# Optimization experiments

Measured on AMD Instinct MI355X. Metric: run time of the kernel, lower is better.

The kernel has to match this reference:

```python
import jax, jax.numpy as jnp
import numpy as np

B = 1024      # graphs
NODES = 128   # nodes per graph (uniform -> batch_ptr = arange(B+1)*NODES)
IN = 64
HID = 256
OUT = 128
NBLK = 3
TAU = 0.25


def _ln(x, g, b):
    # LayerNorm over last dim, eps=1e-5 (torch default)
    mu = jnp.mean(x, axis=-1, keepdims=True)
    var = jnp.mean((x - mu) ** 2, axis=-1, keepdims=True)
    return (x - mu) / jnp.sqrt(var + 1e-5) * g + b


def setup_inputs() -> dict:
    key = jax.random.key(0)
    ks = jax.random.split(key, 4)
    sc = 0.05
    return {
        "H": jax.random.normal(ks[0], (B * NODES, IN), jnp.float32),
        "batch_ptr": jnp.arange(B + 1, dtype=jnp.int32) * NODES,
        # ResNetMLP params: stem Linear(IN->HID)+LN, NBLK residual blocks
        # Linear(HID->HID)+LN+ReLU, head Linear(HID->OUT)+LN (last_norm=True).
        "W_in": jax.random.normal(ks[1], (IN, HID), jnp.float32) * sc,
        "b_in": jnp.zeros((HID,), jnp.float32),
        "g_in": jnp.ones((HID,), jnp.float32),
        "beta_in": jnp.zeros((HID,), jnp.float32),
        "Wb": jax.random.normal(ks[2], (NBLK, HID, HID), jnp.float32) * sc,
        "bb": jnp.zeros((NBLK, HID), jnp.float32),
        "gb": jnp.ones((NBLK, HID), jnp.float32),
        "betab": jnp.zeros((NBLK, HID), jnp.float32),
        "W_out": jax.random.normal(ks[3], (HID, OUT), jnp.float32) * sc,
        "b_out": jnp.zeros((OUT,), jnp.float32),
        "g_out": jnp.ones((OUT,), jnp.float32),
        "beta_out": jnp.zeros((OUT,), jnp.float32),
    }


def reference(H, batch_ptr, W_in, b_in, g_in, beta_in, Wb, bb, gb, betab,
              W_out, b_out, g_out, beta_out):
    # ResNetMLP projection (dropout is identity in eval)
    x = jax.nn.relu(_ln(H @ W_in + b_in, g_in, beta_in))          # [N, HID]
    for k in range(NBLK):
        x = x + jax.nn.relu(_ln(x @ Wb[k] + bb[k], gb[k], betab[k]))
    z = _ln(x @ W_out + b_out, g_out, beta_out)                   # [N, OUT]

    # Uniform-size graphs: ragged per-graph loop vectorizes to [Bg, n, OUT]
    Bg = batch_ptr.shape[0] - 1
    n = H.shape[0] // Bg
    z3 = z.reshape(Bg, n, OUT)

    # s_i = mean_j ||z_i - z_j||_2 (includes j=i, distance 0)
    sq = jnp.sum(z3 * z3, axis=-1)                                # [Bg, n]
    d2 = sq[:, :, None] + sq[:, None, :] - 2.0 * jnp.einsum("bid,bjd->bij", z3, z3)
    d = jnp.sqrt(jnp.maximum(d2, 0.0) + 1e-12)                    # [Bg, n, n]
    s = jnp.mean(d, axis=-1)                                      # [Bg, n]

    w = jax.nn.softmax(s / TAU, axis=-1)                          # [Bg, n]
    v_loc = jnp.einsum("bi,bid->bd", w, z3)                       # [Bg, OUT]
    return v_loc, w
```

## Files before the change

### kernel.cpp

```cpp
#include <hip/hip_runtime.h>
#include <stdint.h>


typedef __attribute__((ext_vector_type(8))) short bf16x8;
typedef __attribute__((ext_vector_type(4))) float f32x4;

#define XB_STRIDE 264
#define ZB_STRIDE 136

__device__ __forceinline__ unsigned int rne16(float f) {
  unsigned int u = __builtin_bit_cast(unsigned int, f);
  return u + 0x7fffu + ((u >> 16) & 1u);
}
__device__ __forceinline__ unsigned short f2bf(float f) {
  return (unsigned short)(rne16(f) >> 16);
}
__device__ __forceinline__ float bf2f(unsigned short h) {
  unsigned int u = ((unsigned int)h) << 16;
  return __builtin_bit_cast(float, u);
}
__device__ __forceinline__ f32x4 zero4() {
  f32x4 v; v.x = 0.f; v.y = 0.f; v.z = 0.f; v.w = 0.f; return v;
}
__device__ __forceinline__ unsigned int pack_pair(float v) {
  unsigned int t = rne16(v);
  unsigned int tp = (unsigned int)__builtin_amdgcn_update_dpp(
      0, (int)t, 0xB1, 0xF, 0xF, true);
  return __builtin_amdgcn_perm(tp, t, 0x07060302);
}
template <int CTRL>
__device__ __forceinline__ float dpp_add(float v) {
  int p = __builtin_amdgcn_update_dpp(0, __builtin_bit_cast(int, v),
                                      CTRL, 0xF, 0xF, true);
  return v + __builtin_bit_cast(float, p);
}
__device__ __forceinline__ float red16(float v) {
  v = dpp_add<0xB1>(v);
  v = dpp_add<0x4E>(v);
  v = dpp_add<0x141>(v);
  v = dpp_add<0x140>(v);
  return v;
}

__global__ void prep_weights(const float* __restrict__ Win, const float* __restrict__ Wb,
                             const float* __restrict__ Wout, unsigned short* __restrict__ ws) {
  int g = blockIdx.x * 256 + threadIdx.x;
  if (g >= 30720) return;
  const float* W; int N; int local;
  if (g < 2048) { W = Win; N = 256; local = g; }
  else if (g < 26624) {
    int i = g - 2048; int blk = i >> 13; local = i & 8191;
    W = Wb + blk * 65536; N = 256;
  } else { W = Wout; N = 128; local = g - 26624; }
  int f = local >> 6, lane = local & 63;
  int NTL = N >> 4;
  int kc = f / NTL, ntile = f - kc * NTL;
  int n = ntile * 16 + (lane & 15);
  int k0 = kc * 32 + (lane >> 4) * 8;
  unsigned short o[8];
#pragma unroll
  for (int e = 0; e < 8; ++e) o[e] = f2bf(W[(size_t)(k0 + e) * N + n]);
  *reinterpret_cast<uint4*>(ws + (size_t)g * 8) = *reinterpret_cast<uint4*>(o);
}

template <int KL, int N, int MODE>
__device__ __forceinline__ void layer(unsigned short* __restrict__ Xb,
                                      float* __restrict__ statQ, float* __restrict__ muR,
                                      const unsigned short* __restrict__ Wf,
                                      int tid, int wave, int lane,
                                      const float* __restrict__ bias,
                                      const float* __restrict__ gam,
                                      const float* __restrict__ bet,
                                      f32x4 (&xprev)[2][2]) {
  constexpr int NT = N / 128;
  constexpr int NTL = N / 16;
  constexpr int KC = KL / 32;
  const int q = lane >> 4, l16 = lane & 15;
  const int colbase = wave * 16 * NT;
  const unsigned short* Wl = Wf + lane * 8;

  float bcol[NT], gcol[NT], becol[NT];
#pragma unroll
  for (int nt = 0; nt < NT; ++nt) {
    int col = colbase + 16 * nt + l16;
    bcol[nt] = bias[col]; gcol[nt] = gam[col]; becol[nt] = bet[col];
  }
  f32x4 acc[2][NT];
#pragma unroll
  for (int mt = 0; mt < 2; ++mt)
#pragma unroll
    for (int nt = 0; nt < NT; ++nt) acc[mt][nt] = zero4();

  bf16x8 bcur[NT];
#pragma unroll
  for (int nt = 0; nt < NT; ++nt)
    bcur[nt] = *reinterpret_cast<const bf16x8*>(Wl + (size_t)(wave * NT + nt) * 512);

  __syncthreads();
#pragma unroll
  for (int kc = 0; kc < KC; ++kc) {
    bf16x8 bnext[NT];
    if (kc + 1 < KC) {
#pragma unroll
      for (int nt = 0; nt < NT; ++nt)
        bnext[nt] = *reinterpret_cast<const bf16x8*>(
            Wl + (size_t)((kc + 1) * NTL + wave * NT + nt) * 512);
    }
    const int kk = kc * 32 + q * 8;
    bf16x8 a0 = *reinterpret_cast<const bf16x8*>(Xb + l16 * XB_STRIDE + kk);
    bf16x8 a1 = *reinterpret_cast<const bf16x8*>(Xb + (16 + l16) * XB_STRIDE + kk);
#pragma unroll
    for (int nt = 0; nt < NT; ++nt)
      acc[0][nt] = __builtin_amdgcn_mfma_f32_16x16x32_bf16(a0, bcur[nt], acc[0][nt], 0, 0, 0);
#pragma unroll
    for (int nt = 0; nt < NT; ++nt)
      acc[1][nt] = __builtin_amdgcn_mfma_f32_16x16x32_bf16(a1, bcur[nt], acc[1][nt], 0, 0, 0);
    if (kc + 1 < KC) {
#pragma unroll
      for (int nt = 0; nt < NT; ++nt) bcur[nt] = bnext[nt];
    }
  }

#pragma unroll
  for (int mt = 0; mt < 2; ++mt) {
#pragma unroll
    for (int nt = 0; nt < NT; ++nt) {
      acc[mt][nt].x += bcol[nt]; acc[mt][nt].y += bcol[nt];
      acc[mt][nt].z += bcol[nt]; acc[mt][nt].w += bcol[nt];
    }
    f32x4 s1 = acc[mt][0];
    f32x4 s2 = acc[mt][0] * acc[mt][0];
    if constexpr (NT == 2) { s1 += acc[mt][1]; s2 += acc[mt][1] * acc[mt][1]; }
#pragma unroll
    for (int r = 0; r < 4; ++r) { s1[r] = red16(s1[r]); s2[r] = red16(s2[r]); }
    if (l16 == 0) {
      float* sp = statQ + wave * 68 + mt * 32 + q * 8;
      f32x4 v0, v1;
      v0.x = s1.x; v0.y = s2.x; v0.z = s1.y; v0.w = s2.y;
      v1.x = s1.z; v1.y = s2.z; v1.z = s1.w; v1.w = s2.w;
      *reinterpret_cast<f32x4*>(sp) = v0;
      *reinterpret_cast<f32x4*>(sp + 4) = v1;
    }
  }
  __syncthreads();
  if (tid < 32) {
    float S1 = 0.f, S2 = 0.f;
#pragma unroll
    for (int w = 0; w < 8; ++w) {
      float2 v = *reinterpret_cast<const float2*>(statQ + w * 68 + 2 * tid);
      S1 += v.x; S2 += v.y;
    }
    float mu = S1 * (1.0f / N);
    float var = S2 * (1.0f / N) - mu * mu;
    float rstd = rsqrtf(var + 1e-5f);
    float2 o; o.x = mu; o.y = rstd;
    *reinterpret_cast<float2*>(muR + 2 * tid) = o;
  }
  __syncthreads();
  unsigned int* Xw = reinterpret_cast<unsigned int*>(Xb);
#pragma unroll
  for (int mt = 0; mt < 2; ++mt)
#pragma unroll
    for (int r = 0; r < 4; ++r) {
      const int row = 16 * mt + 4 * q + r;
      float2 m = *reinterpret_cast<const float2*>(muR + 2 * row);
      const float nmr = -m.x * m.y;
#pragma unroll
      for (int nt = 0; nt < NT; ++nt) {
        float z = __builtin_fmaf(acc[mt][nt][r], m.y, nmr);
        float o = __builtin_fmaf(z, gcol[nt], becol[nt]);
        float xv;
        if constexpr (MODE == 0) { xv = fmaxf(o, 0.f); xprev[mt][nt][r] = xv; }
        else if constexpr (MODE == 1) {
          xv = xprev[mt][nt][r] + fmaxf(o, 0.f); xprev[mt][nt][r] = xv;
        } else { xv = o; }
        unsigned int pk = pack_pair(xv);
        if ((l16 & 1) == 0)
          Xw[row * 132 + ((colbase + 16 * nt + l16) >> 1)] = pk;
      }
    }
}

__global__ __attribute__((amdgpu_flat_work_group_size(512, 512), amdgpu_waves_per_eu(4)))
void mlp_main(const float* __restrict__ H, const unsigned short* __restrict__ ws,
              const float* __restrict__ b_in, const float* __restrict__ g_in,
              const float* __restrict__ beta_in,
              const float* __restrict__ bb, const float* __restrict__ gb,
              const float* __restrict__ betab,
              const float* __restrict__ b_out, const float* __restrict__ g_out,
              const float* __restrict__ beta_out,
              unsigned short* __restrict__ Z) {
  __shared__ __attribute__((aligned(16))) unsigned short Xb[32 * XB_STRIDE];
  __shared__ __attribute__((aligned(16))) float statQ[8 * 68];
  __shared__ __attribute__((aligned(16))) float muR[64];
  const int tid = threadIdx.x;
  const int wave = tid >> 6, lane = tid & 63;

  {
    int row = tid >> 4, c4 = (tid & 15) * 4;
    float4 f = *reinterpret_cast<const float4*>(
        H + ((size_t)blockIdx.x * 32 + row) * 64 + c4);
    unsigned int t0 = rne16(f.x), t1 = rne16(f.y), t2 = rne16(f.z), t3 = rne16(f.w);
    uint2 o;
    o.x = __builtin_amdgcn_perm(t1, t0, 0x07060302);
    o.y = __builtin_amdgcn_perm(t3, t2, 0x07060302);
    *reinterpret_cast<uint2*>(Xb + row * XB_STRIDE + c4) = o;
  }

  f32x4 xprev[2][2];
  layer<64, 256, 0>(Xb, statQ, muR, ws,           tid, wave, lane, b_in,     g_in,     beta_in,  xprev);
  layer<256, 256, 1>(Xb, statQ, muR, ws + 16384,  tid, wave, lane, bb,       gb,       betab,    xprev);
  layer<256, 256, 1>(Xb, statQ, muR, ws + 81920,  tid, wave, lane, bb + 256, gb + 256, betab + 256, xprev);
  layer<256, 256, 1>(Xb, statQ, muR, ws + 147456, tid, wave, lane, bb + 512, gb + 512, betab + 512, xprev);
  layer<256, 128, 2>(Xb, statQ, muR, ws + 212992, tid, wave, lane, b_out,    g_out,    beta_out, xprev);
  __syncthreads();

  {
    int row = tid >> 4, c8 = (tid & 15) * 8;
    uint4 v = *reinterpret_cast<const uint4*>(Xb + row * XB_STRIDE + c8);
    *reinterpret_cast<uint4*>(Z + ((size_t)blockIdx.x * 32 + row) * 128 + c8) = v;
  }
}

__global__ __attribute__((amdgpu_flat_work_group_size(512, 512)))
void pool_main(const unsigned short* __restrict__ Z, float* __restrict__ out) {
  __shared__ unsigned short Zb[128 * ZB_STRIDE];
  __shared__ float sqv[128], sm[128], smw[128];
  const int tid = threadIdx.x;
  const int g = blockIdx.x;
  const int wave = tid >> 6, lane = tid & 63;
  const int q = lane >> 4, l16 = lane & 15;

  {
    int zr = tid >> 2, zc = (tid & 3) * 32;
    const uint4* zp = reinterpret_cast<const uint4*>(Z + ((size_t)g * 128 + zr) * 128 + zc);
    uint4* zd = reinterpret_cast<uint4*>(Zb + zr * ZB_STRIDE + zc);
    zd[0] = zp[0]; zd[1] = zp[1]; zd[2] = zp[2]; zd[3] = zp[3];
  }
  __syncthreads();

  f32x4 g2[8];
#pragma unroll
  for (int nt = 0; nt < 8; ++nt) g2[nt] = zero4();
#pragma unroll
  for (int ks = 0; ks < 4; ++ks) {
    int kk = ks * 32 + q * 8;
    bf16x8 a = *reinterpret_cast<const bf16x8*>(Zb + (16 * wave + l16) * ZB_STRIDE + kk);
#pragma unroll
    for (int nt = 0; nt < 8; ++nt) {
      bf16x8 bfr = *reinterpret_cast<const bf16x8*>(Zb + (16 * nt + l16) * ZB_STRIDE + kk);
      g2[nt] = __builtin_amdgcn_mfma_f32_16x16x32_bf16(a, bfr, g2[nt], 0, 0, 0);
    }
  }
  if ((l16 >> 2) == q) {
#pragma unroll
    for (int nt = 0; nt < 8; ++nt)
      if (nt == wave) {
#pragma unroll
        for (int r = 0; r < 4; ++r)
          if ((l16 & 3) == r) sqv[16 * wave + l16] = g2[nt][r];
      }
  }
  __syncthreads();
  float sqi[4];
#pragma unroll
  for (int r = 0; r < 4; ++r) sqi[r] = sqv[16 * wave + q * 4 + r];
  float sp[4] = {0.f, 0.f, 0.f, 0.f};
#pragma unroll
  for (int nt = 0; nt < 8; ++nt) {
    float sqj = sqv[16 * nt + l16];
#pragma unroll
    for (int r = 0; r < 4; ++r) {
      float d2 = sqi[r] + sqj - 2.0f * g2[nt][r];
      sp[r] += sqrtf(fmaxf(d2, 0.f) + 1e-12f);
    }
  }
#pragma unroll
  for (int d = 1; d < 16; d <<= 1) {
#pragma unroll
    for (int r = 0; r < 4; ++r) { float t = sp[r]; t += __shfl_xor(t, d); sp[r] = t; }
  }
  if (l16 == 0) {
#pragma unroll
    for (int r = 0; r < 4; ++r) sm[16 * wave + q * 4 + r] = sp[r] * (1.0f / 128.0f);
  }
  __syncthreads();
  if (wave == 0) {
    float l0 = sm[lane] * 4.0f;
    float l1 = sm[lane + 64] * 4.0f;
    float mx = fmaxf(l0, l1);
#pragma unroll
    for (int d = 1; d < 64; d <<= 1) mx = fmaxf(mx, __shfl_xor(mx, d));
    float e0 = __expf(l0 - mx), e1 = __expf(l1 - mx);
    float ss = e0 + e1;
#pragma unroll
    for (int d = 1; d < 64; d <<= 1) ss += __shfl_xor(ss, d);
    float inv = 1.0f / ss;
    float w0 = e0 * inv, w1 = e1 * inv;
    smw[lane] = w0;
    smw[lane + 64] = w1;
    out[131072 + g * 128 + lane] = w0;
    out[131072 + g * 128 + 64 + lane] = w1;
  }
  __syncthreads();
  {
    int c = 16 * wave + l16;
    float acv = 0.f;
#pragma unroll
    for (int i0 = 0; i0 < 32; ++i0) {
      int i = q * 32 + i0;
      acv += smw[i] * bf2f(Zb[i * ZB_STRIDE + c]);
    }
    acv += __shfl_xor(acv, 16);
    acv += __shfl_xor(acv, 32);
    if (q == 0) out[g * 128 + c] = acv;
  }
}

extern "C" void kernel_launch(void* const* d_in, const int* in_sizes, int n_in,
                              void* d_out, int out_size, void* d_ws, size_t ws_size,
                              hipStream_t stream) {
  (void)in_sizes; (void)n_in; (void)out_size; (void)ws_size;
  const float* H        = (const float*)d_in[0];
  const float* W_in     = (const float*)d_in[2];
  const float* b_in     = (const float*)d_in[3];
  const float* g_in     = (const float*)d_in[4];
  const float* beta_in  = (const float*)d_in[5];
  const float* Wb       = (const float*)d_in[6];
  const float* bb       = (const float*)d_in[7];
  const float* gb       = (const float*)d_in[8];
  const float* betab    = (const float*)d_in[9];
  const float* W_out    = (const float*)d_in[10];
  const float* b_out    = (const float*)d_in[11];
  const float* g_out    = (const float*)d_in[12];
  const float* beta_out = (const float*)d_in[13];
  float* out = (float*)d_out;
  unsigned short* ws = (unsigned short*)d_ws;
  unsigned short* Z = ws + 262144;

  prep_weights<<<120, 256, 0, stream>>>(W_in, Wb, W_out, ws);
  mlp_main<<<4096, 512, 0, stream>>>(H, ws, b_in, g_in, beta_in,
                                     bb, gb, betab, b_out, g_out, beta_out, Z);
  pool_main<<<1024, 512, 0, stream>>>(Z, out);
}
```

Before: 251.1 us.

## Fuse MLP and per-graph pooling into one 1024-thread kernel per graph

Merges the MLP kernel and the pooling kernel into a single kernel, with one 1024-thread block per graph handling all 128 rows. The 16 waves are arranged as 4 row-groups by 4 column-groups, so each wave computes a 32x64 tile. The final bf16 Z activations stay in LDS for the distance/softmax/pooling stage, which removes the Z round trip through global memory and one launch. In exchange LDS per block grows to about 70KB, occupancy drops to fewer blocks per CU, and half the waves sit idle during pooling.

```diff
diff --git a/kernel.cpp b/kernel.cpp
--- a/kernel.cpp
+++ b/kernel.cpp
@@ -6,7 +6,6 @@
 typedef __attribute__((ext_vector_type(4))) float f32x4;
 
 #define XB_STRIDE 264
-#define ZB_STRIDE 136
 
 __device__ __forceinline__ unsigned int rne16(float f) {
   unsigned int u = __builtin_bit_cast(unsigned int, f);
@@ -71,13 +70,51 @@
                                       const float* __restrict__ bias,
                                       const float* __restrict__ gam,
                                       const float* __restrict__ bet,
-                                      f32x4 (&xprev)[2][2]) {
-  constexpr int NT = N / 128;
+                                      f32x4 (&xprev)[2][4]) {
+  constexpr int NT = N / 64;
   constexpr int NTL = N / 16;
   constexpr int KC = KL / 32;
+  const int wr = wave >> 2, wc = wave & 3;
   const int q = lane >> 4, l16 = lane & 15;
-  const int colbase = wave * 16 * NT;
+  const int rowbase = wr * 32;
+  const int colbase = wc * 16 * NT;
   const unsigned short* Wl = Wf + lane * 8;
+
+  f32x4 acc[2][NT];
+#pragma unroll
+  for (int mt = 0; mt < 2; ++mt)
+#pragma unroll
+    for (int nt = 0; nt < NT; ++nt) acc[mt][nt] = zero4();
+
+  bf16x8 bcur[NT];
+#pragma unroll
+  for (int nt = 0; nt < NT; ++nt)
+    bcur[nt] = *reinterpret_cast<const bf16x8*>(Wl + (size_t)(wc * NT + nt) * 512);
+
+  __syncthreads();
+#pragma unroll
+  for (int kc = 0; kc < KC; ++kc) {
+    bf16x8 bnext[NT];
+    if (kc + 1 < KC) {
+#pragma unroll
+      for (int nt = 0; nt < NT; ++nt)
+        bnext[nt] = *reinterpret_cast<const bf16x8*>(
+            Wl + (size_t)((kc + 1) * NTL + wc * NT + nt) * 512);
+    }
+    const int kk = kc * 32 + q * 8;
+    bf16x8 a0 = *reinterpret_cast<const bf16x8*>(Xb + (rowbase + l16) * XB_STRIDE + kk);
+    bf16x8 a1 = *reinterpret_cast<const bf16x8*>(Xb + (rowbase + 16 + l16) * XB_STRIDE + kk);
+#pragma unroll
+    for (int nt = 0; nt < NT; ++nt)
+      acc[0][nt] = __builtin_amdgcn_mfma_f32_16x16x32_bf16(a0, bcur[nt], acc[0][nt], 0, 0, 0);
+#pragma unroll
+    for (int nt = 0; nt < NT; ++nt)
+      acc[1][nt] = __builtin_amdgcn_mfma_f32_16x16x32_bf16(a1, bcur[nt], acc[1][nt], 0, 0, 0);
+    if (kc + 1 < KC) {
+#pragma unroll
+      for (int nt = 0; nt < NT; ++nt) bcur[nt] = bnext[nt];
+    }
+  }
 
   float bcol[NT], gcol[NT], becol[NT];
 #pragma unroll
@@ -85,42 +122,6 @@
     int col = colbase + 16 * nt + l16;
     bcol[nt] = bias[col]; gcol[nt] = gam[col]; becol[nt] = bet[col];
   }
-  f32x4 acc[2][NT];
-#pragma unroll
-  for (int mt = 0; mt < 2; ++mt)
-#pragma unroll
-    for (int nt = 0; nt < NT; ++nt) acc[mt][nt] = zero4();
-
-  bf16x8 bcur[NT];
-#pragma unroll
-  for (int nt = 0; nt < NT; ++nt)
-    bcur[nt] = *reinterpret_cast<const bf16x8*>(Wl + (size_t)(wave * NT + nt) * 512);
-
-  __syncthreads();
-#pragma unroll
-  for (int kc = 0; kc < KC; ++kc) {
-    bf16x8 bnext[NT];
-    if (kc + 1 < KC) {
-#pragma unroll
-      for (int nt = 0; nt < NT; ++nt)
-        bnext[nt] = *reinterpret_cast<const bf16x8*>(
-            Wl + (size_t)((kc + 1) * NTL + wave * NT + nt) * 512);
-    }
-    const int kk = kc * 32 + q * 8;
-    bf16x8 a0 = *reinterpret_cast<const bf16x8*>(Xb + l16 * XB_STRIDE + kk);
-    bf16x8 a1 = *reinterpret_cast<const bf16x8*>(Xb + (16 + l16) * XB_STRIDE + kk);
-#pragma unroll
-    for (int nt = 0; nt < NT; ++nt)
-      acc[0][nt] = __builtin_amdgcn_mfma_f32_16x16x32_bf16(a0, bcur[nt], acc[0][nt], 0, 0, 0);
-#pragma unroll
-    for (int nt = 0; nt < NT; ++nt)
-      acc[1][nt] = __builtin_amdgcn_mfma_f32_16x16x32_bf16(a1, bcur[nt], acc[1][nt], 0, 0, 0);
-    if (kc + 1 < KC) {
-#pragma unroll
-      for (int nt = 0; nt < NT; ++nt) bcur[nt] = bnext[nt];
-    }
-  }
-
 #pragma unroll
   for (int mt = 0; mt < 2; ++mt) {
 #pragma unroll
@@ -130,24 +131,25 @@
     }
     f32x4 s1 = acc[mt][0];
     f32x4 s2 = acc[mt][0] * acc[mt][0];
-    if constexpr (NT == 2) { s1 += acc[mt][1]; s2 += acc[mt][1] * acc[mt][1]; }
+#pragma unroll
+    for (int nt = 1; nt < NT; ++nt) { s1 += acc[mt][nt]; s2 += acc[mt][nt] * acc[mt][nt]; }
 #pragma unroll
     for (int r = 0; r < 4; ++r) { s1[r] = red16(s1[r]); s2[r] = red16(s2[r]); }
     if (l16 == 0) {
-      float* sp = statQ + wave * 68 + mt * 32 + q * 8;
-      f32x4 v0, v1;
-      v0.x = s1.x; v0.y = s2.x; v0.z = s1.y; v0.w = s2.y;
-      v1.x = s1.z; v1.y = s2.z; v1.z = s1.w; v1.w = s2.w;
-      *reinterpret_cast<f32x4*>(sp) = v0;
-      *reinterpret_cast<f32x4*>(sp + 4) = v1;
-    }
-  }
-  __syncthreads();
-  if (tid < 32) {
+#pragma unroll
+      for (int r = 0; r < 4; ++r) {
+        int row = rowbase + 16 * mt + 4 * q + r;
+        float2 o; o.x = s1[r]; o.y = s2[r];
+        *reinterpret_cast<float2*>(statQ + row * 9 + 2 * wc) = o;
+      }
+    }
+  }
+  __syncthreads();
+  if (tid < 128) {
     float S1 = 0.f, S2 = 0.f;
 #pragma unroll
-    for (int w = 0; w < 8; ++w) {
-      float2 v = *reinterpret_cast<const float2*>(statQ + w * 68 + 2 * tid);
+    for (int w = 0; w < 4; ++w) {
+      float2 v = *reinterpret_cast<const float2*>(statQ + tid * 9 + 2 * w);
       S1 += v.x; S2 += v.y;
     }
     float mu = S1 * (1.0f / N);
@@ -162,7 +164,7 @@
   for (int mt = 0; mt < 2; ++mt)
 #pragma unroll
     for (int r = 0; r < 4; ++r) {
-      const int row = 16 * mt + 4 * q + r;
+      const int row = rowbase + 16 * mt + 4 * q + r;
       float2 m = *reinterpret_cast<const float2*>(muR + 2 * row);
       const float nmr = -m.x * m.y;
 #pragma unroll
@@ -181,33 +183,38 @@
     }
 }
 
-__global__ __attribute__((amdgpu_flat_work_group_size(512, 512), amdgpu_waves_per_eu(4)))
-void mlp_main(const float* __restrict__ H, const unsigned short* __restrict__ ws,
-              const float* __restrict__ b_in, const float* __restrict__ g_in,
-              const float* __restrict__ beta_in,
-              const float* __restrict__ bb, const float* __restrict__ gb,
-              const float* __restrict__ betab,
-              const float* __restrict__ b_out, const float* __restrict__ g_out,
-              const float* __restrict__ beta_out,
-              unsigned short* __restrict__ Z) {
-  __shared__ __attribute__((aligned(16))) unsigned short Xb[32 * XB_STRIDE];
-  __shared__ __attribute__((aligned(16))) float statQ[8 * 68];
-  __shared__ __attribute__((aligned(16))) float muR[64];
+__global__ __attribute__((amdgpu_flat_work_group_size(1024, 1024), amdgpu_waves_per_eu(4)))
+void fused_main(const float* __restrict__ H, const unsigned short* __restrict__ ws,
+                const float* __restrict__ b_in, const float* __restrict__ g_in,
+                const float* __restrict__ beta_in,
+                const float* __restrict__ bb, const float* __restrict__ gb,
+                const float* __restrict__ betab,
+                const float* __restrict__ b_out, const float* __restrict__ g_out,
+                const float* __restrict__ beta_out,
+                float* __restrict__ out) {
+  __shared__ __attribute__((aligned(16))) unsigned short Xb[128 * XB_STRIDE];
+  __shared__ __attribute__((aligned(16))) float statQ[128 * 9 + 8];
+  __shared__ __attribute__((aligned(16))) float muR[256];
+  __shared__ float sqv[128], sm[128], smw[128];
   const int tid = threadIdx.x;
+  const int g = blockIdx.x;
   const int wave = tid >> 6, lane = tid & 63;
+  const int q = lane >> 4, l16 = lane & 15;
 
   {
-    int row = tid >> 4, c4 = (tid & 15) * 4;
-    float4 f = *reinterpret_cast<const float4*>(
-        H + ((size_t)blockIdx.x * 32 + row) * 64 + c4);
-    unsigned int t0 = rne16(f.x), t1 = rne16(f.y), t2 = rne16(f.z), t3 = rne16(f.w);
-    uint2 o;
-    o.x = __builtin_amdgcn_perm(t1, t0, 0x07060302);
-    o.y = __builtin_amdgcn_perm(t3, t2, 0x07060302);
-    *reinterpret_cast<uint2*>(Xb + row * XB_STRIDE + c4) = o;
-  }
-
-  f32x4 xprev[2][2];
+    int row = tid >> 3, c8 = (tid & 7) * 8;
+    const float4* hp = reinterpret_cast<const float4*>(
+        H + ((size_t)g * 128 + row) * 64 + c8);
+    float4 fa = hp[0], fb = hp[1];
+    uint4 o;
+    o.x = __builtin_amdgcn_perm(rne16(fa.y), rne16(fa.x), 0x07060302);
+    o.y = __builtin_amdgcn_perm(rne16(fa.w), rne16(fa.z), 0x07060302);
+    o.z = __builtin_amdgcn_perm(rne16(fb.y), rne16(fb.x), 0x07060302);
+    o.w = __builtin_amdgcn_perm(rne16(fb.w), rne16(fb.z), 0x07060302);
+    *reinterpret_cast<uint4*>(Xb + row * XB_STRIDE + c8) = o;
+  }
+
+  f32x4 xprev[2][4];
   layer<64, 256, 0>(Xb, statQ, muR, ws,           tid, wave, lane, b_in,     g_in,     beta_in,  xprev);
   layer<256, 256, 1>(Xb, statQ, muR, ws + 16384,  tid, wave, lane, bb,       gb,       betab,    xprev);
   layer<256, 256, 1>(Xb, statQ, muR, ws + 81920,  tid, wave, lane, bb + 256, gb + 256, betab + 256, xprev);
@@ -215,74 +222,54 @@
   layer<256, 128, 2>(Xb, statQ, muR, ws + 212992, tid, wave, lane, b_out,    g_out,    beta_out, xprev);
   __syncthreads();
 
-  {
-    int row = tid >> 4, c8 = (tid & 15) * 8;
-    uint4 v = *reinterpret_cast<const uint4*>(Xb + row * XB_STRIDE + c8);
-    *reinterpret_cast<uint4*>(Z + ((size_t)blockIdx.x * 32 + row) * 128 + c8) = v;
-  }
-}
-
-__global__ __attribute__((amdgpu_flat_work_group_size(512, 512)))
-void pool_main(const unsigned short* __restrict__ Z, float* __restrict__ out) {
-  __shared__ unsigned short Zb[128 * ZB_STRIDE];
-  __shared__ float sqv[128], sm[128], smw[128];
-  const int tid = threadIdx.x;
-  const int g = blockIdx.x;
-  const int wave = tid >> 6, lane = tid & 63;
-  const int q = lane >> 4, l16 = lane & 15;
-
-  {
-    int zr = tid >> 2, zc = (tid & 3) * 32;
-    const uint4* zp = reinterpret_cast<const uint4*>(Z + ((size_t)g * 128 + zr) * 128 + zc);
-    uint4* zd = reinterpret_cast<uint4*>(Zb + zr * ZB_STRIDE + zc);
-    zd[0] = zp[0]; zd[1] = zp[1]; zd[2] = zp[2]; zd[3] = zp[3];
-  }
-  __syncthreads();
-
   f32x4 g2[8];
 #pragma unroll
   for (int nt = 0; nt < 8; ++nt) g2[nt] = zero4();
-#pragma unroll
-  for (int ks = 0; ks < 4; ++ks) {
-    int kk = ks * 32 + q * 8;
-    bf16x8 a = *reinterpret_cast<const bf16x8*>(Zb + (16 * wave + l16) * ZB_STRIDE + kk);
+  if (wave < 8) {
+#pragma unroll
+    for (int ks = 0; ks < 4; ++ks) {
+      int kk = ks * 32 + q * 8;
+      bf16x8 a = *reinterpret_cast<const bf16x8*>(Xb + (16 * wave + l16) * XB_STRIDE + kk);
+#pragma unroll
+      for (int nt = 0; nt < 8; ++nt) {
+        bf16x8 bfr = *reinterpret_cast<const bf16x8*>(Xb + (16 * nt + l16) * XB_STRIDE + kk);
+        g2[nt] = __builtin_amdgcn_mfma_f32_16x16x32_bf16(a, bfr, g2[nt], 0, 0, 0);
+      }
+    }
+    if ((l16 >> 2) == q) {
+#pragma unroll
+      for (int nt = 0; nt < 8; ++nt)
+        if (nt == wave) {
+#pragma unroll
+          for (int r = 0; r < 4; ++r)
+            if ((l16 & 3) == r) sqv[16 * wave + l16] = g2[nt][r];
+        }
+    }
+  }
+  __syncthreads();
+  if (wave < 8) {
+    float sqi[4];
+#pragma unroll
+    for (int r = 0; r < 4; ++r) sqi[r] = sqv[16 * wave + q * 4 + r];
+    float sp[4] = {0.f, 0.f, 0.f, 0.f};
 #pragma unroll
     for (int nt = 0; nt < 8; ++nt) {
-      bf16x8 bfr = *reinterpret_cast<const bf16x8*>(Zb + (16 * nt + l16) * ZB_STRIDE + kk);
-      g2[nt] = __builtin_amdgcn_mfma_f32_16x16x32_bf16(a, bfr, g2[nt], 0, 0, 0);
-    }
-  }
-  if ((l16 >> 2) == q) {
-#pragma unroll
-    for (int nt = 0; nt < 8; ++nt)
-      if (nt == wave) {
-#pragma unroll
-        for (int r = 0; r < 4; ++r)
-          if ((l16 & 3) == r) sqv[16 * wave + l16] = g2[nt][r];
+      float sqj = sqv[16 * nt + l16];
+#pragma unroll
+      for (int r = 0; r < 4; ++r) {
+        float d2 = sqi[r] + sqj - 2.0f * g2[nt][r];
+        sp[r] += sqrtf(fmaxf(d2, 0.f) + 1e-12f);
       }
-  }
-  __syncthreads();
-  float sqi[4];
-#pragma unroll
-  for (int r = 0; r < 4; ++r) sqi[r] = sqv[16 * wave + q * 4 + r];
-  float sp[4] = {0.f, 0.f, 0.f, 0.f};
-#pragma unroll
-  for (int nt = 0; nt < 8; ++nt) {
-    float sqj = sqv[16 * nt + l16];
-#pragma unroll
-    for (int r = 0; r < 4; ++r) {
-      float d2 = sqi[r] + sqj - 2.0f * g2[nt][r];
-      sp[r] += sqrtf(fmaxf(d2, 0.f) + 1e-12f);
-    }
-  }
-#pragma unroll
-  for (int d = 1; d < 16; d <<= 1) {
-#pragma unroll
-    for (int r = 0; r < 4; ++r) { float t = sp[r]; t += __shfl_xor(t, d); sp[r] = t; }
-  }
-  if (l16 == 0) {
-#pragma unroll
-    for (int r = 0; r < 4; ++r) sm[16 * wave + q * 4 + r] = sp[r] * (1.0f / 128.0f);
+    }
+#pragma unroll
+    for (int d = 1; d < 16; d <<= 1) {
+#pragma unroll
+      for (int r = 0; r < 4; ++r) { float t = sp[r]; t += __shfl_xor(t, d); sp[r] = t; }
+    }
+    if (l16 == 0) {
+#pragma unroll
+      for (int r = 0; r < 4; ++r) sm[16 * wave + q * 4 + r] = sp[r] * (1.0f / 128.0f);
+    }
   }
   __syncthreads();
   if (wave == 0) {
@@ -303,13 +290,13 @@
     out[131072 + g * 128 + 64 + lane] = w1;
   }
   __syncthreads();
-  {
+  if (wave < 8) {
     int c = 16 * wave + l16;
     float acv = 0.f;
 #pragma unroll
     for (int i0 = 0; i0 < 32; ++i0) {
       int i = q * 32 + i0;
-      acv += smw[i] * bf2f(Zb[i * ZB_STRIDE + c]);
+      acv += smw[i] * bf2f(Xb[i * XB_STRIDE + c]);
     }
     acv += __shfl_xor(acv, 16);
     acv += __shfl_xor(acv, 32);
@@ -336,10 +323,8 @@
   const float* beta_out = (const float*)d_in[13];
   float* out = (float*)d_out;
   unsigned short* ws = (unsigned short*)d_ws;
-  unsigned short* Z = ws + 262144;
 
   prep_weights<<<120, 256, 0, stream>>>(W_in, Wb, W_out, ws);
-  mlp_main<<<4096, 512, 0, stream>>>(H, ws, b_in, g_in, beta_in,
-                                     bb, gb, betab, b_out, g_out, beta_out, Z);
-  pool_main<<<1024, 512, 0, stream>>>(Z, out);
-}
+  fused_main<<<1024, 1024, 0, stream>>>(H, ws, b_in, g_in, beta_in,
+                                        bb, gb, betab, b_out, g_out, beta_out, out);
+}
```

Measured after the change: 492.5 us. 1.96x slower.

## Stage MLP accumulators in LDS and do LayerNorm row-wise with larger blocks

Applied to the files above, without the earlier changes.

Each MLP block now covers 64 rows with 1024 threads, arranged as 2 row groups by 8 column groups of waves. MFMA accumulators go to an fp32 LDS tile, and each row's LayerNorm is computed by 16 lanes that own contiguous columns. This replaces the cross-wave statistics exchange (the statQ/muR passes and an extra barrier), lets bias/gamma/beta be loaded once into LDS, and writes the final layer straight to global memory. In exchange it uses about 103 KB of dynamic LDS per block, which limits residency to one large block per CU and adds an LDS round trip of fp32 data each layer.

```diff
diff --git a/kernel.cpp b/kernel.cpp
--- a/kernel.cpp
+++ b/kernel.cpp
@@ -6,7 +6,11 @@
 typedef __attribute__((ext_vector_type(4))) float f32x4;
 
 #define XB_STRIDE 264
+#define YB_STRIDE 260
 #define ZB_STRIDE 136
+#define LDS_YB    33792
+#define LDS_PAR   100352
+#define LDS_TOTAL 103424
 
 __device__ __forceinline__ unsigned int rne16(float f) {
   unsigned int u = __builtin_bit_cast(unsigned int, f);
@@ -21,12 +25,6 @@
 }
 __device__ __forceinline__ f32x4 zero4() {
   f32x4 v; v.x = 0.f; v.y = 0.f; v.z = 0.f; v.w = 0.f; return v;
-}
-__device__ __forceinline__ unsigned int pack_pair(float v) {
-  unsigned int t = rne16(v);
-  unsigned int tp = (unsigned int)__builtin_amdgcn_update_dpp(
-      0, (int)t, 0xB1, 0xF, 0xF, true);
-  return __builtin_amdgcn_perm(tp, t, 0x07060302);
 }
 template <int CTRL>
 __device__ __forceinline__ float dpp_add(float v) {
@@ -65,26 +63,24 @@
 
 template <int KL, int N, int MODE>
 __device__ __forceinline__ void layer(unsigned short* __restrict__ Xb,
-                                      float* __restrict__ statQ, float* __restrict__ muR,
+                                      float* __restrict__ Yb, float* __restrict__ par,
                                       const unsigned short* __restrict__ Wf,
                                       int tid, int wave, int lane,
                                       const float* __restrict__ bias,
                                       const float* __restrict__ gam,
                                       const float* __restrict__ bet,
-                                      f32x4 (&xprev)[2][2]) {
+                                      float (&xprev)[16],
+                                      unsigned short* __restrict__ Z, size_t rowglob) {
   constexpr int NT = N / 128;
   constexpr int NTL = N / 16;
   constexpr int KC = KL / 32;
+  constexpr int CPT = N / 16;
+  const int wr = wave >> 3, wc = wave & 7;
   const int q = lane >> 4, l16 = lane & 15;
-  const int colbase = wave * 16 * NT;
+  const int rowbase = wr * 32;
+  const int colbase = wc * 16 * NT;
   const unsigned short* Wl = Wf + lane * 8;
 
-  float bcol[NT], gcol[NT], becol[NT];
-#pragma unroll
-  for (int nt = 0; nt < NT; ++nt) {
-    int col = colbase + 16 * nt + l16;
-    bcol[nt] = bias[col]; gcol[nt] = gam[col]; becol[nt] = bet[col];
-  }
   f32x4 acc[2][NT];
 #pragma unroll
   for (int mt = 0; mt < 2; ++mt)
@@ -94,9 +90,13 @@
   bf16x8 bcur[NT];
 #pragma unroll
   for (int nt = 0; nt < NT; ++nt)
-    bcur[nt] = *reinterpret_cast<const bf16x8*>(Wl + (size_t)(wave * NT + nt) * 512);
-
-  __syncthreads();
+    bcur[nt] = *reinterpret_cast<const bf16x8*>(Wl + (size_t)(wc * NT + nt) * 512);
+
+  __syncthreads();
+  if (tid < 3 * N) {
+    float v = (tid < N) ? bias[tid] : (tid < 2 * N) ? gam[tid - N] : bet[tid - 2 * N];
+    par[tid] = v;
+  }
 #pragma unroll
   for (int kc = 0; kc < KC; ++kc) {
     bf16x8 bnext[NT];
@@ -104,11 +104,11 @@
 #pragma unroll
       for (int nt = 0; nt < NT; ++nt)
         bnext[nt] = *reinterpret_cast<const bf16x8*>(
-            Wl + (size_t)((kc + 1) * NTL + wave * NT + nt) * 512);
+            Wl + (size_t)((kc + 1) * NTL + wc * NT + nt) * 512);
     }
     const int kk = kc * 32 + q * 8;
-    bf16x8 a0 = *reinterpret_cast<const bf16x8*>(Xb + l16 * XB_STRIDE + kk);
-    bf16x8 a1 = *reinterpret_cast<const bf16x8*>(Xb + (16 + l16) * XB_STRIDE + kk);
+    bf16x8 a0 = *reinterpret_cast<const bf16x8*>(Xb + (rowbase + l16) * XB_STRIDE + kk);
+    bf16x8 a1 = *reinterpret_cast<const bf16x8*>(Xb + (rowbase + 16 + l16) * XB_STRIDE + kk);
 #pragma unroll
     for (int nt = 0; nt < NT; ++nt)
       acc[0][nt] = __builtin_amdgcn_mfma_f32_16x16x32_bf16(a0, bcur[nt], acc[0][nt], 0, 0, 0);
@@ -122,66 +122,69 @@
   }
 
 #pragma unroll
-  for (int mt = 0; mt < 2; ++mt) {
+  for (int mt = 0; mt < 2; ++mt)
 #pragma unroll
     for (int nt = 0; nt < NT; ++nt) {
-      acc[mt][nt].x += bcol[nt]; acc[mt][nt].y += bcol[nt];
-      acc[mt][nt].z += bcol[nt]; acc[mt][nt].w += bcol[nt];
-    }
-    f32x4 s1 = acc[mt][0];
-    f32x4 s2 = acc[mt][0] * acc[mt][0];
-    if constexpr (NT == 2) { s1 += acc[mt][1]; s2 += acc[mt][1] * acc[mt][1]; }
-#pragma unroll
-    for (int r = 0; r < 4; ++r) { s1[r] = red16(s1[r]); s2[r] = red16(s2[r]); }
-    if (l16 == 0) {
-      float* sp = statQ + wave * 68 + mt * 32 + q * 8;
-      f32x4 v0, v1;
-      v0.x = s1.x; v0.y = s2.x; v0.z = s1.y; v0.w = s2.y;
-      v1.x = s1.z; v1.y = s2.z; v1.z = s1.w; v1.w = s2.w;
-      *reinterpret_cast<f32x4*>(sp) = v0;
-      *reinterpret_cast<f32x4*>(sp + 4) = v1;
-    }
-  }
-  __syncthreads();
-  if (tid < 32) {
-    float S1 = 0.f, S2 = 0.f;
-#pragma unroll
-    for (int w = 0; w < 8; ++w) {
-      float2 v = *reinterpret_cast<const float2*>(statQ + w * 68 + 2 * tid);
-      S1 += v.x; S2 += v.y;
-    }
-    float mu = S1 * (1.0f / N);
-    float var = S2 * (1.0f / N) - mu * mu;
-    float rstd = rsqrtf(var + 1e-5f);
-    float2 o; o.x = mu; o.y = rstd;
-    *reinterpret_cast<float2*>(muR + 2 * tid) = o;
-  }
-  __syncthreads();
-  unsigned int* Xw = reinterpret_cast<unsigned int*>(Xb);
-#pragma unroll
-  for (int mt = 0; mt < 2; ++mt)
-#pragma unroll
-    for (int r = 0; r < 4; ++r) {
-      const int row = 16 * mt + 4 * q + r;
-      float2 m = *reinterpret_cast<const float2*>(muR + 2 * row);
-      const float nmr = -m.x * m.y;
-#pragma unroll
-      for (int nt = 0; nt < NT; ++nt) {
-        float z = __builtin_fmaf(acc[mt][nt][r], m.y, nmr);
-        float o = __builtin_fmaf(z, gcol[nt], becol[nt]);
-        float xv;
-        if constexpr (MODE == 0) { xv = fmaxf(o, 0.f); xprev[mt][nt][r] = xv; }
-        else if constexpr (MODE == 1) {
-          xv = xprev[mt][nt][r] + fmaxf(o, 0.f); xprev[mt][nt][r] = xv;
-        } else { xv = o; }
-        unsigned int pk = pack_pair(xv);
-        if ((l16 & 1) == 0)
-          Xw[row * 132 + ((colbase + 16 * nt + l16) >> 1)] = pk;
-      }
-    }
-}
-
-__global__ __attribute__((amdgpu_flat_work_group_size(512, 512), amdgpu_waves_per_eu(4)))
+      const int col = colbase + 16 * nt + l16;
+#pragma unroll
+      for (int r = 0; r < 4; ++r)
+        Yb[(rowbase + 16 * mt + 4 * q + r) * YB_STRIDE + col] = acc[mt][nt][r];
+    }
+  __syncthreads();
+
+  const int row = wave * 4 + q;
+  const int c0 = l16 * CPT;
+  float y[CPT];
+#pragma unroll
+  for (int j = 0; j < CPT / 4; ++j)
+    *reinterpret_cast<f32x4*>(y + 4 * j) =
+        *reinterpret_cast<const f32x4*>(Yb + row * YB_STRIDE + c0 + 4 * j);
+  float bv[CPT], gv[CPT], ev[CPT];
+#pragma unroll
+  for (int j = 0; j < CPT / 4; ++j) {
+    *reinterpret_cast<f32x4*>(bv + 4 * j) = *reinterpret_cast<const f32x4*>(par + c0 + 4 * j);
+    *reinterpret_cast<f32x4*>(gv + 4 * j) = *reinterpret_cast<const f32x4*>(par + N + c0 + 4 * j);
+    *reinterpret_cast<f32x4*>(ev + 4 * j) = *reinterpret_cast<const f32x4*>(par + 2 * N + c0 + 4 * j);
+  }
+  float s1 = 0.f, s2 = 0.f;
+#pragma unroll
+  for (int e = 0; e < CPT; ++e) {
+    y[e] += bv[e];
+    s1 += y[e]; s2 = __builtin_fmaf(y[e], y[e], s2);
+  }
+  s1 = red16(s1); s2 = red16(s2);
+  const float mu = s1 * (1.0f / N);
+  const float var = s2 * (1.0f / N) - mu * mu;
+  const float rstd = rsqrtf(var + 1e-5f);
+  const float nmr = -mu * rstd;
+  unsigned int pk[CPT / 2];
+#pragma unroll
+  for (int e = 0; e < CPT; ++e) {
+    float t = __builtin_fmaf(y[e], rstd, nmr);
+    float o = __builtin_fmaf(t, gv[e], ev[e]);
+    float xv;
+    if constexpr (MODE == 0) { xv = fmaxf(o, 0.f); xprev[e] = xv; }
+    else if constexpr (MODE == 1) { xv = xprev[e] + fmaxf(o, 0.f); xprev[e] = xv; }
+    else { xv = o; }
+    if (e & 1)
+      pk[e >> 1] = __builtin_amdgcn_perm(rne16(xv), rne16(__builtin_bit_cast(float, pk[e >> 1])),
+                                         0x07060302);
+    else
+      pk[e >> 1] = __builtin_bit_cast(unsigned int, xv);
+  }
+  if constexpr (MODE != 2) {
+    unsigned int* Xw = reinterpret_cast<unsigned int*>(Xb);
+#pragma unroll
+    for (int j = 0; j < CPT / 8; ++j)
+      *reinterpret_cast<uint4*>(Xw + row * 132 + (c0 >> 1) + 4 * j) =
+          *reinterpret_cast<uint4*>(pk + 4 * j);
+  } else {
+    *reinterpret_cast<uint4*>(Z + (rowglob + row) * 128 + c0) =
+        *reinterpret_cast<uint4*>(pk);
+  }
+}
+
+__global__ __attribute__((amdgpu_flat_work_group_size(1024, 1024), amdgpu_waves_per_eu(4)))
 void mlp_main(const float* __restrict__ H, const unsigned short* __restrict__ ws,
               const float* __restrict__ b_in, const float* __restrict__ g_in,
               const float* __restrict__ beta_in,
@@ -190,36 +193,29 @@
               const float* __restrict__ b_out, const float* __restrict__ g_out,
               const float* __restrict__ beta_out,
               unsigned short* __restrict__ Z) {
-  __shared__ __attribute__((aligned(16))) unsigned short Xb[32 * XB_STRIDE];
-  __shared__ __attribute__((aligned(16))) float statQ[8 * 68];
-  __shared__ __attribute__((aligned(16))) float muR[64];
+  extern __shared__ char smem[];
+  unsigned short* Xb = (unsigned short*)smem;
+  float* Yb = (float*)(smem + LDS_YB);
+  float* par = (float*)(smem + LDS_PAR);
   const int tid = threadIdx.x;
   const int wave = tid >> 6, lane = tid & 63;
+  const size_t rowglob = (size_t)blockIdx.x * 64;
 
   {
     int row = tid >> 4, c4 = (tid & 15) * 4;
-    float4 f = *reinterpret_cast<const float4*>(
-        H + ((size_t)blockIdx.x * 32 + row) * 64 + c4);
-    unsigned int t0 = rne16(f.x), t1 = rne16(f.y), t2 = rne16(f.z), t3 = rne16(f.w);
+    float4 f = *reinterpret_cast<const float4*>(H + (rowglob + row) * 64 + c4);
     uint2 o;
-    o.x = __builtin_amdgcn_perm(t1, t0, 0x07060302);
-    o.y = __builtin_amdgcn_perm(t3, t2, 0x07060302);
+    o.x = __builtin_amdgcn_perm(rne16(f.y), rne16(f.x), 0x07060302);
+    o.y = __builtin_amdgcn_perm(rne16(f.w), rne16(f.z), 0x07060302);
     *reinterpret_cast<uint2*>(Xb + row * XB_STRIDE + c4) = o;
   }
 
-  f32x4 xprev[2][2];
-  layer<64, 256, 0>(Xb, statQ, muR, ws,           tid, wave, lane, b_in,     g_in,     beta_in,  xprev);
-  layer<256, 256, 1>(Xb, statQ, muR, ws + 16384,  tid, wave, lane, bb,       gb,       betab,    xprev);
-  layer<256, 256, 1>(Xb, statQ, muR, ws + 81920,  tid, wave, lane, bb + 256, gb + 256, betab + 256, xprev);
-  layer<256, 256, 1>(Xb, statQ, muR, ws + 147456, tid, wave, lane, bb + 512, gb + 512, betab + 512, xprev);
-  layer<256, 128, 2>(Xb, statQ, muR, ws + 212992, tid, wave, lane, b_out,    g_out,    beta_out, xprev);
-  __syncthreads();
-
-  {
-    int row = tid >> 4, c8 = (tid & 15) * 8;
-    uint4 v = *reinterpret_cast<const uint4*>(Xb + row * XB_STRIDE + c8);
-    *reinterpret_cast<uint4*>(Z + ((size_t)blockIdx.x * 32 + row) * 128 + c8) = v;
-  }
+  float xprev[16];
+  layer<64, 256, 0>(Xb, Yb, par, ws,           tid, wave, lane, b_in,     g_in,     beta_in,  xprev, Z, rowglob);
+  layer<256, 256, 1>(Xb, Yb, par, ws + 16384,  tid, wave, lane, bb,       gb,       betab,    xprev, Z, rowglob);
+  layer<256, 256, 1>(Xb, Yb, par, ws + 81920,  tid, wave, lane, bb + 256, gb + 256, betab + 256, xprev, Z, rowglob);
+  layer<256, 256, 1>(Xb, Yb, par, ws + 147456, tid, wave, lane, bb + 512, gb + 512, betab + 512, xprev, Z, rowglob);
+  layer<256, 128, 2>(Xb, Yb, par, ws + 212992, tid, wave, lane, b_out,    g_out,    beta_out, xprev, Z, rowglob);
 }
 
 __global__ __attribute__((amdgpu_flat_work_group_size(512, 512)))
@@ -339,7 +335,9 @@
   unsigned short* Z = ws + 262144;
 
   prep_weights<<<120, 256, 0, stream>>>(W_in, Wb, W_out, ws);
-  mlp_main<<<4096, 512, 0, stream>>>(H, ws, b_in, g_in, beta_in,
-                                     bb, gb, betab, b_out, g_out, beta_out, Z);
+  hipFuncSetAttribute(reinterpret_cast<const void*>(mlp_main),
+                      hipFuncAttributeMaxDynamicSharedMemorySize, LDS_TOTAL);
+  mlp_main<<<2048, 1024, LDS_TOTAL, stream>>>(H, ws, b_in, g_in, beta_in,
+                                              bb, gb, betab, b_out, g_out, beta_out, Z);
   pool_main<<<1024, 512, 0, stream>>>(Z, out);
 }
```

Result: no change. 255.4 us (+1.7%).
